# Kernel tuning notes

Hardware: AMD Instinct MI355X
Metric: run time of the kernel (lower is better)

The kernel has to match this reference:

```python
import jax, jax.numpy as jnp
import numpy as np

HEADS, HID, OUT_C, IN_C = 8, 128, 2, 64
D = HID // HEADS
NODE = {"cell0": 50000, "cell1": 100000, "cell2": 25000}
# (src_type, dst_type, edge_name, num_edges)
ETYPES = [("cell0", "cell0", "u00", 200000),
          ("cell1", "cell1", "u11", 200000),
          ("cell1", "cell0", "b10", 100000),
          ("cell2", "cell1", "b21", 50000)]


def _segment_softmax(scores, seg, num_segments):
    # numerically-stable softmax over irregular destination segments
    m = jax.ops.segment_max(scores, seg, num_segments=num_segments)
    e = jnp.exp(scores - m[seg])
    s = jax.ops.segment_sum(e, seg, num_segments=num_segments)
    return e / (s[seg] + 1e-16)


def setup_inputs() -> dict:
    key = jax.random.key(0)
    ks = iter(jax.random.split(key, 64))
    s = 0.1
    inp = {}
    for nt, n in NODE.items():
        inp[f"x_{nt}"] = jax.random.normal(next(ks), (n, IN_C), jnp.float32)
    for st, dt, name, e in ETYPES:
        src = jax.random.randint(next(ks), (e,), 0, NODE[st], jnp.int32)
        dst = jax.random.randint(next(ks), (e,), 0, NODE[dt], jnp.int32)
        inp[f"ei_{name}"] = jnp.stack([src, dst])
    # HANConv params: per node-type projection, per edge-type attention vectors
    for nt in NODE:
        inp[f"W_{nt}"] = jax.random.normal(next(ks), (IN_C, HID), jnp.float32) * s
        inp[f"b_{nt}"] = jnp.zeros((HID,), jnp.float32)
    for _, _, name, _ in ETYPES:
        inp[f"as_{name}"] = jax.random.normal(next(ks), (HEADS, D), jnp.float32) * s
        inp[f"ad_{name}"] = jax.random.normal(next(ks), (HEADS, D), jnp.float32) * s
    # semantic attention params + final classifier
    inp["k_w"] = jax.random.normal(next(ks), (HID, HID), jnp.float32) * s
    inp["k_b"] = jnp.zeros((HID,), jnp.float32)
    inp["q"] = jax.random.normal(next(ks), (HID,), jnp.float32) * s
    inp["lin_w"] = jax.random.normal(next(ks), (HID, OUT_C), jnp.float32) * s
    inp["lin_b"] = jnp.zeros((OUT_C,), jnp.float32)
    return inp


def _han_conv(x, ei, W, b, att_s, att_d, k_w, k_b, q):
    # node-level: project each node type -> [N, H, D]
    h = {nt: (x[nt] @ W[nt] + b[nt]).reshape(-1, HEADS, D) for nt in NODE}
    outs = {nt: [] for nt in NODE}
    for st, dt, name, _ in ETYPES:
        xs, xd = h[st], h[dt]
        a_s = (xs * att_s[name]).sum(-1)  # [Ns, H]
        a_d = (xd * att_d[name]).sum(-1)  # [Nd, H]
        src, dst = ei[name][0], ei[name][1]
        alpha = jax.nn.leaky_relu(a_s[src] + a_d[dst], 0.2)  # [E, H]
        alpha = _segment_softmax(alpha, dst, NODE[dt])
        msg = xs[src] * alpha[:, :, None]  # [E, H, D]
        agg = jax.ops.segment_sum(msg, dst, num_segments=NODE[dt])
        outs[dt].append(jax.nn.relu(agg.reshape(-1, HID)))
    # semantic-level attention across metapaths per dst node type
    res = {}
    for nt, lst in outs.items():
        if not lst:
            res[nt] = None
            continue
        stk = jnp.stack(lst)  # [M, N, HID]
        score = (q * jnp.tanh(stk @ k_w + k_b).mean(1)).sum(-1)  # [M]
        attn = jax.nn.softmax(score)
        res[nt] = jnp.einsum('m,mnf->nf', attn, stk)
    return res


def reference(x_cell0, x_cell1, x_cell2,
              W_cell0, b_cell0, W_cell1, b_cell1, W_cell2, b_cell2,
              as_u00, ad_u00, as_u11, ad_u11, as_b10, ad_b10, as_b21, ad_b21,
              k_w, k_b, q, lin_w, lin_b,
              ei_u00, ei_u11, ei_b10, ei_b21):
    x = {"cell0": x_cell0, "cell1": x_cell1, "cell2": x_cell2}
    ei = {"u00": ei_u00, "u11": ei_u11, "b10": ei_b10, "b21": ei_b21}
    W = {"cell0": W_cell0, "cell1": W_cell1, "cell2": W_cell2}
    b = {"cell0": b_cell0, "cell1": b_cell1, "cell2": b_cell2}
    att_s = {"u00": as_u00, "u11": as_u11, "b10": as_b10, "b21": as_b21}
    att_d = {"u00": ad_u00, "u11": ad_u11, "b10": ad_b10, "b21": ad_b21}
    # HAN.forward calls han_conv twice with identical inputs (first result
    # discarded); in eval mode (dropout off) both calls are identical math,
    # so we compute it once.
    out = _han_conv(x, ei, W, b, att_s, att_d, k_w, k_b, q)
    pooled = sum(jnp.sum(v, axis=0) for v in out.values() if v is not None)  # global_add_pool, batch=None
    return jax.nn.sigmoid(pooled[None, :] @ lin_w + lin_b)  # [1, OUT_C]
```

## Files before the change

### kernel.cpp

```cpp
#include <hip/hip_runtime.h>
#include <hip/hip_fp16.h>

#define N0 50000
#define N1 100000
#define N2 25000
#define E00 200000
#define E11 200000
#define E10 100000
#define E21 50000
#define EE  550000
#define ND  300000
#define NB  293
#define NT_ALL 18750
#define HID 128
#define INC 64

typedef _Float16 half8 __attribute__((ext_vector_type(8)));
typedef _Float16 half4_t __attribute__((ext_vector_type(4)));
typedef float float4v __attribute__((ext_vector_type(4)));
typedef float floatx2 __attribute__((ext_vector_type(2)));

struct PrepT {
    const float* W; const float* bias;
    const float* av0; const float* av1; const float* av2; const float* av3;
    _Float16* wtg; _Float16* adtg; float* bdc;
};

__device__ __forceinline__ void decode_edge(
    int e, const int* ei00, const int* ei10, const int* ei11, const int* ei21,
    int& src, int& slot)
{
    if (e < E00)                    { src = ei00[e];               slot = ei00[E00 + e]; }
    else if (e < E00 + E10)         { int i = e - E00;             src = ei10[i]; slot = 50000  + ei10[E10 + i]; }
    else if (e < E00 + E10 + E11)   { int i = e - E00 - E10;       src = ei11[i]; slot = 100000 + ei11[E11 + i]; }
    else                            { int i = e - E00 - E10 - E11; src = ei21[i]; slot = 200000 + ei21[E21 + i]; }
}

__global__ __launch_bounds__(256) void prep_kernel(
    PrepT p0, PrepT p1, PrepT p2,
    const float* __restrict__ kw, const float* __restrict__ lw,
    unsigned char* __restrict__ kwf8,
    const int* __restrict__ ei00, const int* __restrict__ ei10,
    const int* __restrict__ ei11, const int* __restrict__ ei21,
    int* __restrict__ cnt)
{
    if (blockIdx.x >= 32) {
        int e = (blockIdx.x - 32) * 256 + threadIdx.x;
        if (e >= EE) return;
        int src, slot;
        decode_edge(e, ei00, ei10, ei11, ei21, src, slot);
        atomicAdd(&cnt[slot], 1);
        return;
    }
    if (blockIdx.x >= 24) {
        int base = (blockIdx.x - 24) * 256 + threadIdx.x;
        for (int it = 0; it < 9; ++it) {
            int idx = base + it * 2048;
            int f = idx >> 7, g = idx & 127;
            float v;
            if (f < 128)      v = kw[g * 128 + f];
            else if (f < 130) v = lw[g * 2 + (f - 128)];
            else              v = 0.f;
            int r = __builtin_amdgcn_cvt_pk_fp8_f32(v, 0.f, 0, false);
            kwf8[idx] = (unsigned char)r;
        }
        return;
    }
    PrepT P = (blockIdx.x >= 16) ? p2 : (blockIdx.x >= 8) ? p1 : p0;
    const int lb = blockIdx.x & 7;
    const int t2 = lb * 256 + threadIdx.x;
    {
        int f = t2 >> 4, g0 = (t2 & 15) * 4;
        half4_t v;
#pragma unroll
        for (int j = 0; j < 4; ++j) v[j] = (_Float16)P.W[(g0 + j) * 128 + f];
        *(half4_t*)&P.wtg[f * 64 + g0] = v;
    }
    {
        int c = t2 >> 6, g = t2 & 63;
        const float* av = (c < 8) ? P.av0 : (c < 16) ? P.av1 : (c < 24) ? P.av2 : P.av3;
        float v = 0.f;
        if (av) {
            int hh = c & 7;
#pragma unroll
            for (int d = 0; d < 16; ++d)
                v += P.W[g * 128 + hh * 16 + d] * av[hh * 16 + d];
        }
        P.adtg[c * 64 + g] = (_Float16)v;
    }
    if (lb == 0 && threadIdx.x < 32) {
        int c = threadIdx.x;
        const float* av = (c < 8) ? P.av0 : (c < 16) ? P.av1 : (c < 24) ? P.av2 : P.av3;
        float v = 0.f;
        if (av) {
            int hh = c & 7;
#pragma unroll
            for (int d = 0; d < 16; ++d)
                v += P.bias[hh * 16 + d] * av[hh * 16 + d];
        }
        P.bdc[c] = v;
    }
}

struct PT {
    const float* x; const float* bias; unsigned char* h;
    float* ao0; float* ao1; float* ao2; float* ao3;
    const _Float16* wtg; const _Float16* adtg; const float* bdc;
    int N; int ntiles; int bstart; int nblocks;
};

#define HPAD 136
#define PROJ_BLKS 1024

__global__ __launch_bounds__(256, 2) void proj_mfma(
    PT t0, PT t1, PT t2,
    const int* __restrict__ cnt, int* __restrict__ part)
{
    __shared__ _Float16 ht[4][16][HPAD];
    __shared__ int swt[4];
    const int tid = threadIdx.x;
    const int lane = tid & 63, wv = tid >> 6;
    const int fi = lane & 15, hi = lane >> 4;

    if (blockIdx.x >= PROJ_BLKS) {
        const int b = blockIdx.x - PROJ_BLKS;
        int i0 = b * 1024 + tid * 4;
        int s = 0;
#pragma unroll
        for (int k = 0; k < 4; ++k) { int i = i0 + k; s += (i < ND) ? cnt[i] : 0; }
#pragma unroll
        for (int off = 1; off < 64; off <<= 1) s += __shfl_xor(s, off);
        if ((tid & 63) == 0) swt[tid >> 6] = s;
        __syncthreads();
        if (tid == 0) part[b] = swt[0] + swt[1] + swt[2] + swt[3];
        return;
    }

    PT A = (blockIdx.x >= t2.bstart) ? t2 : (blockIdx.x >= t1.bstart) ? t1 : t0;

    half8 bfr[8][2], bd[2][2];
#pragma unroll
    for (int nt = 0; nt < 8; ++nt)
#pragma unroll
        for (int kb = 0; kb < 2; ++kb)
            bfr[nt][kb] = *(const half8*)&A.wtg[(nt * 16 + fi) * 64 + kb * 32 + hi * 8];
#pragma unroll
    for (int t = 0; t < 2; ++t)
#pragma unroll
        for (int kb = 0; kb < 2; ++kb)
            bd[t][kb] = *(const half8*)&A.adtg[(t * 16 + fi) * 64 + kb * 32 + hi * 8];

    float bvv[8];
#pragma unroll
    for (int nt = 0; nt < 8; ++nt) bvv[nt] = A.bias[nt * 16 + fi];
    const float bdc0 = A.bdc[fi];
    const float bdc1 = A.bdc[16 + fi];

    float* aolo = (fi >= 8) ? A.ao1 : A.ao0;
    float* aohi = (fi >= 8) ? A.ao3 : A.ao2;
    const bool has_hi = (A.ao2 != nullptr) || (A.ao3 != nullptr);

    const int stride = A.nblocks * 4;
    for (int t = (blockIdx.x - A.bstart) * 4 + wv; t < A.ntiles; t += stride) {
        const int base = t * 16;
        int rsrc = base + fi; if (rsrc >= A.N) rsrc = A.N - 1;
        const float* xp = A.x + (size_t)rsrc * 64 + hi * 8;
        float4 u0 = *(const float4*)(xp);
        float4 u1 = *(const float4*)(xp + 4);
        float4 u2 = *(const float4*)(xp + 32);
        float4 u3 = *(const float4*)(xp + 36);
        half8 a0, a1;
        a0[0] = (_Float16)u0.x; a0[1] = (_Float16)u0.y; a0[2] = (_Float16)u0.z; a0[3] = (_Float16)u0.w;
        a0[4] = (_Float16)u1.x; a0[5] = (_Float16)u1.y; a0[6] = (_Float16)u1.z; a0[7] = (_Float16)u1.w;
        a1[0] = (_Float16)u2.x; a1[1] = (_Float16)u2.y; a1[2] = (_Float16)u2.z; a1[3] = (_Float16)u2.w;
        a1[4] = (_Float16)u3.x; a1[5] = (_Float16)u3.y; a1[6] = (_Float16)u3.z; a1[7] = (_Float16)u3.w;

        float4v c[8];
#pragma unroll
        for (int nt = 0; nt < 8; ++nt) {
            float4v z = {0.f, 0.f, 0.f, 0.f};
            z = __builtin_amdgcn_mfma_f32_16x16x32_f16(a0, bfr[nt][0], z, 0, 0, 0);
            z = __builtin_amdgcn_mfma_f32_16x16x32_f16(a1, bfr[nt][1], z, 0, 0, 0);
            c[nt] = z;
        }
        float4v d0 = {0.f, 0.f, 0.f, 0.f};
        d0 = __builtin_amdgcn_mfma_f32_16x16x32_f16(a0, bd[0][0], d0, 0, 0, 0);
        d0 = __builtin_amdgcn_mfma_f32_16x16x32_f16(a1, bd[0][1], d0, 0, 0, 0);
        float4v d1 = {0.f, 0.f, 0.f, 0.f};
        if (has_hi) {
            d1 = __builtin_amdgcn_mfma_f32_16x16x32_f16(a0, bd[1][0], d1, 0, 0, 0);
            d1 = __builtin_amdgcn_mfma_f32_16x16x32_f16(a1, bd[1][1], d1, 0, 0, 0);
        }

#pragma unroll
        for (int nt = 0; nt < 8; ++nt)
#pragma unroll
            for (int r = 0; r < 4; ++r)
                ht[wv][hi * 4 + r][nt * 16 + fi] = (_Float16)(c[nt][r] + bvv[nt]);
#pragma unroll
        for (int i = 0; i < 4; ++i) {
            int row = i * 4 + hi;
            int node = base + row;
            if (node < A.N) {
                half8 v = *(const half8*)&ht[wv][row][fi * 8];
                int pa = __builtin_amdgcn_cvt_pk_fp8_f32((float)v[0], (float)v[1], 0, false);
                pa = __builtin_amdgcn_cvt_pk_fp8_f32((float)v[2], (float)v[3], pa, true);
                int pb = __builtin_amdgcn_cvt_pk_fp8_f32((float)v[4], (float)v[5], 0, false);
                pb = __builtin_amdgcn_cvt_pk_fp8_f32((float)v[6], (float)v[7], pb, true);
                int2 o = {pa, pb};
                *(int2*)(A.h + (size_t)node * 128 + fi * 8) = o;
            }
        }
        if (aolo) {
#pragma unroll
            for (int r = 0; r < 4; ++r) {
                int node = base + hi * 4 + r;
                if (node < A.N) aolo[(size_t)node * 8 + (fi & 7)] = d0[r] + bdc0;
            }
        }
        if (aohi) {
#pragma unroll
            for (int r = 0; r < 4; ++r) {
                int node = base + hi * 4 + r;
                if (node < A.N) aohi[(size_t)node * 8 + (fi & 7)] = d1[r] + bdc1;
            }
        }
    }
}

__global__ __launch_bounds__(256) void scan23_kernel(
    const int* __restrict__ cnt, const int* __restrict__ part,
    int* __restrict__ off, int* __restrict__ cursor)
{
    __shared__ int sd[256];
    __shared__ int pex[512];
    __shared__ int wt[4];
    const int tid = threadIdx.x, b = blockIdx.x;
    const int lane = tid & 63, wv = tid >> 6;

    int p0 = (2 * tid     < NB) ? part[2 * tid]     : 0;
    int p1 = (2 * tid + 1 < NB) ? part[2 * tid + 1] : 0;
    int ps = p0 + p1;
    sd[tid] = ps; __syncthreads();
    for (int d = 1; d < 256; d <<= 1) {
        int v = (tid >= d) ? sd[tid - d] : 0;
        __syncthreads();
        sd[tid] += v;
        __syncthreads();
    }
    int exc = sd[tid] - ps;
    pex[2 * tid] = exc;
    pex[2 * tid + 1] = exc + p0;
    __syncthreads();

    int i0 = b * 1024 + tid * 4;
    int v[4];
#pragma unroll
    for (int k = 0; k < 4; ++k) { int i = i0 + k; v[k] = (i < ND) ? cnt[i] : 0; }
    int ts = v[0] + v[1] + v[2] + v[3];
    int inc = ts;
#pragma unroll
    for (int d = 1; d < 64; d <<= 1) {
        int u = __shfl_up(inc, d);
        if (lane >= d) inc += u;
    }
    int wexc = inc - ts;
    if (lane == 63) wt[wv] = inc;
    __syncthreads();
    int wbase = 0;
    for (int w = 0; w < wv; ++w) wbase += wt[w];
    int base = pex[b] + wbase + wexc;
    int pre = 0;
#pragma unroll
    for (int k = 0; k < 4; ++k) {
        int i = i0 + k;
        if (i < ND) { off[i] = base + pre; cursor[i] = base + pre; }
        pre += v[k];
    }
}

__global__ __launch_bounds__(256) void fill_kernel(
    const int* __restrict__ ei00, const int* __restrict__ ei10,
    const int* __restrict__ ei11, const int* __restrict__ ei21,
    const float* __restrict__ as00, const float* __restrict__ ad00,
    const float* __restrict__ as10, const float* __restrict__ ad10,
    const float* __restrict__ as11, const float* __restrict__ ad11,
    const float* __restrict__ as21, const float* __restrict__ ad21,
    int* __restrict__ cursor, int* __restrict__ srcs, _Float16* __restrict__ wgt)
{
    int e = blockIdx.x * 256 + threadIdx.x;
    if (e >= EE) return;
    int src, d, slot;
    const float* asp; const float* adp;
    if (e < E00) {
        src = ei00[e]; d = ei00[E00 + e]; slot = d; asp = as00; adp = ad00;
    } else if (e < E00 + E10) {
        int i = e - E00; src = ei10[i]; d = ei10[E10 + i]; slot = 50000 + d; asp = as10; adp = ad10;
    } else if (e < E00 + E10 + E11) {
        int i = e - E00 - E10; src = ei11[i]; d = ei11[E11 + i]; slot = 100000 + d; asp = as11; adp = ad11;
    } else {
        int i = e - E00 - E10 - E11; src = ei21[i]; d = ei21[E21 + i]; slot = 200000 + d; asp = as21; adp = ad21;
    }
    float4 sa0 = *(const float4*)(asp + (size_t)src * 8);
    float4 sa1 = *(const float4*)(asp + (size_t)src * 8 + 4);
    float4 da0 = *(const float4*)(adp + (size_t)d * 8);
    float4 da1 = *(const float4*)(adp + (size_t)d * 8 + 4);
    float vv[8] = {sa0.x + da0.x, sa0.y + da0.y, sa0.z + da0.z, sa0.w + da0.w,
                   sa1.x + da1.x, sa1.y + da1.y, sa1.z + da1.z, sa1.w + da1.w};
    half8 w;
#pragma unroll
    for (int h = 0; h < 8; ++h) {
        float v = vv[h];
        v = v > 0.f ? v : 0.2f * v;
        w[h] = (_Float16)__expf(v);
    }
    int pos = atomicAdd(&cursor[slot], 1);
    srcs[pos] = src;
    *(half8*)(wgt + (size_t)pos * 8) = w;
}

__global__ __launch_bounds__(256) void gather_kernel(
    const int* __restrict__ cnt, const int* __restrict__ off,
    const int* __restrict__ srcs, const _Float16* __restrict__ wgt,
    const unsigned char* __restrict__ h0, const unsigned char* __restrict__ h1,
    const unsigned char* __restrict__ h2,
    unsigned char* __restrict__ agg)
{
    const int gid = blockIdx.x * 256 + threadIdx.x;
    const int lane = gid & 63;
    const int g8 = lane >> 3, sub = lane & 7;
    const int slot = (gid >> 6) * 8 + g8;
    const unsigned char* hs = (slot < 50000) ? h0 : (slot < 200000) ? h1 : h2;
    const int deg = cnt[slot], st = off[slot];

    int degm = deg;
    degm = max(degm, __shfl_xor(degm, 8));
    degm = max(degm, __shfl_xor(degm, 16));
    degm = max(degm, __shfl_xor(degm, 32));

    float acc[16];
#pragma unroll
    for (int j = 0; j < 16; ++j) acc[j] = 0.f;
    float sw = 0.f;

    int i = 0;
    for (; i + 2 <= degm; i += 2) {
        bool a0 = (i < deg), a1 = (i + 1 < deg);
        int s0 = 0, s1 = 0;
        if (a0) s0 = srcs[st + i];
        if (a1) s1 = srcs[st + i + 1];
        float w0 = 0.f, w1 = 0.f;
        int4 v0 = {0, 0, 0, 0}, v1 = {0, 0, 0, 0};
        if (a0) { w0 = (float)wgt[(size_t)(st + i) * 8 + sub];
                  v0 = *(const int4*)(hs + (size_t)s0 * 128 + sub * 16); }
        if (a1) { w1 = (float)wgt[(size_t)(st + i + 1) * 8 + sub];
                  v1 = *(const int4*)(hs + (size_t)s1 * 128 + sub * 16); }
        const int wa[4] = {v0.x, v0.y, v0.z, v0.w};
        const int wb[4] = {v1.x, v1.y, v1.z, v1.w};
#pragma unroll
        for (int k = 0; k < 4; ++k) {
            floatx2 fa0 = __builtin_amdgcn_cvt_pk_f32_fp8(wa[k], false);
            floatx2 fa1 = __builtin_amdgcn_cvt_pk_f32_fp8(wa[k], true);
            floatx2 fb0 = __builtin_amdgcn_cvt_pk_f32_fp8(wb[k], false);
            floatx2 fb1 = __builtin_amdgcn_cvt_pk_f32_fp8(wb[k], true);
            acc[4 * k + 0] += w0 * fa0.x + w1 * fb0.x;
            acc[4 * k + 1] += w0 * fa0.y + w1 * fb0.y;
            acc[4 * k + 2] += w0 * fa1.x + w1 * fb1.x;
            acc[4 * k + 3] += w0 * fa1.y + w1 * fb1.y;
        }
        sw += w0 + w1;
    }
    if (i < degm) {
        bool a0 = (i < deg);
        int s0 = 0;
        if (a0) s0 = srcs[st + i];
        float w0 = 0.f;
        int4 v0 = {0, 0, 0, 0};
        if (a0) { w0 = (float)wgt[(size_t)(st + i) * 8 + sub];
                  v0 = *(const int4*)(hs + (size_t)s0 * 128 + sub * 16); }
        const int wa[4] = {v0.x, v0.y, v0.z, v0.w};
#pragma unroll
        for (int k = 0; k < 4; ++k) {
            floatx2 fa0 = __builtin_amdgcn_cvt_pk_f32_fp8(wa[k], false);
            floatx2 fa1 = __builtin_amdgcn_cvt_pk_f32_fp8(wa[k], true);
            acc[4 * k + 0] += w0 * fa0.x;
            acc[4 * k + 1] += w0 * fa0.y;
            acc[4 * k + 2] += w0 * fa1.x;
            acc[4 * k + 3] += w0 * fa1.y;
        }
        sw += w0;
    }

    float rr = __builtin_amdgcn_rcpf(sw + 1e-16f);
    int4 o;
    int pk[4];
#pragma unroll
    for (int k = 0; k < 4; ++k) {
        float r0 = fmaxf(acc[4 * k + 0] * rr, 0.f);
        float r1 = fmaxf(acc[4 * k + 1] * rr, 0.f);
        float r2 = fmaxf(acc[4 * k + 2] * rr, 0.f);
        float r3 = fmaxf(acc[4 * k + 3] * rr, 0.f);
        int p = __builtin_amdgcn_cvt_pk_fp8_f32(r0, r1, 0, false);
        p = __builtin_amdgcn_cvt_pk_fp8_f32(r2, r3, p, true);
        pk[k] = p;
    }
    o.x = pk[0]; o.y = pk[1]; o.z = pk[2]; o.w = pk[3];
    *(int4*)(agg + (size_t)slot * 128 + sub * 16) = o;
}

__global__ __launch_bounds__(256, 2) void semantic_kernel(
    const unsigned char* __restrict__ agg, const unsigned char* __restrict__ kwf8,
    const float* __restrict__ kb, const float* __restrict__ q,
    const float* __restrict__ lb,
    float* __restrict__ cs2, float* __restrict__ score,
    unsigned int* __restrict__ done, float* __restrict__ out)
{
    __shared__ float redv[12];
    const int tid = threadIdx.x;
    const int lane = tid & 63, wv = tid >> 6;
    const int fi = lane & 15, hi = lane >> 4;

    if (tid < 12) redv[tid] = 0.f;
    __syncthreads();

    long bf[9][4];
#pragma unroll
    for (int ft = 0; ft < 9; ++ft)
#pragma unroll
        for (int kk = 0; kk < 4; ++kk)
            bf[ft][kk] = *(const long*)&kwf8[(ft * 16 + fi) * 128 + kk * 32 + hi * 8];

    float qv[8], kbv[8];
#pragma unroll
    for (int ft = 0; ft < 8; ++ft) {
        qv[ft] = q[ft * 16 + fi];
        kbv[ft] = kb[ft * 16 + fi];
    }

    float sc[4] = {0.f, 0.f, 0.f, 0.f};
    float cs[4] = {0.f, 0.f, 0.f, 0.f};
    const int wid = blockIdx.x * 4 + wv;
    const int nw = gridDim.x * 4;

    long af[4] = {0, 0, 0, 0};
    int t = wid;
    if (t < NT_ALL) {
        const unsigned char* rowp = agg + ((size_t)(t * 16 + fi) * 128 + hi * 8);
        af[0] = *(const long*)(rowp);
        af[1] = *(const long*)(rowp + 32);
        af[2] = *(const long*)(rowp + 64);
        af[3] = *(const long*)(rowp + 96);
    }
    while (t < NT_ALL) {
        const int tn = t + nw;
        long afn[4] = {0, 0, 0, 0};
        if (tn < NT_ALL) {
            const unsigned char* rowp = agg + ((size_t)(tn * 16 + fi) * 128 + hi * 8);
            afn[0] = *(const long*)(rowp);
            afn[1] = *(const long*)(rowp + 32);
            afn[2] = *(const long*)(rowp + 64);
            afn[3] = *(const long*)(rowp + 96);
        }
        const int m = (t >= 12500) ? 3 : (t >= 6250) ? 2 : (t >= 3125) ? 1 : 0;
        float tsc = 0.f, tcs;
#pragma unroll
        for (int ft = 0; ft < 8; ++ft) {
            float4v c = {0.f, 0.f, 0.f, 0.f};
            c = __builtin_amdgcn_mfma_f32_16x16x32_fp8_fp8(af[0], bf[ft][0], c, 0, 0, 0);
            c = __builtin_amdgcn_mfma_f32_16x16x32_fp8_fp8(af[1], bf[ft][1], c, 0, 0, 0);
            c = __builtin_amdgcn_mfma_f32_16x16x32_fp8_fp8(af[2], bf[ft][2], c, 0, 0, 0);
            c = __builtin_amdgcn_mfma_f32_16x16x32_fp8_fp8(af[3], bf[ft][3], c, 0, 0, 0);
#pragma unroll
            for (int r = 0; r < 4; ++r) {
                float y = c[r] + kbv[ft];
                float e = __expf(2.f * y);
                tsc += qv[ft] * (1.f - 2.f * __builtin_amdgcn_rcpf(e + 1.f));
            }
        }
        {
            float4v c = {0.f, 0.f, 0.f, 0.f};
            c = __builtin_amdgcn_mfma_f32_16x16x32_fp8_fp8(af[0], bf[8][0], c, 0, 0, 0);
            c = __builtin_amdgcn_mfma_f32_16x16x32_fp8_fp8(af[1], bf[8][1], c, 0, 0, 0);
            c = __builtin_amdgcn_mfma_f32_16x16x32_fp8_fp8(af[2], bf[8][2], c, 0, 0, 0);
            c = __builtin_amdgcn_mfma_f32_16x16x32_fp8_fp8(af[3], bf[8][3], c, 0, 0, 0);
            tcs = c[0] + c[1] + c[2] + c[3];
        }
        if (m == 0)      { sc[0] += tsc; cs[0] += tcs; }
        else if (m == 1) { sc[1] += tsc; cs[1] += tcs; }
        else if (m == 2) { sc[2] += tsc; cs[2] += tcs; }
        else             { sc[3] += tsc; cs[3] += tcs; }
        t = tn;
        af[0] = afn[0]; af[1] = afn[1]; af[2] = afn[2]; af[3] = afn[3];
    }

#pragma unroll
    for (int m = 0; m < 4; ++m) {
        float s = sc[m];
#pragma unroll
        for (int off = 1; off < 64; off <<= 1) s += __shfl_xor(s, off);
        if (lane == 0 && s != 0.f) atomicAdd(&redv[m], s);
        float v = cs[m];
        v += __shfl_xor(v, 16);
        v += __shfl_xor(v, 32);
        if (hi == 0 && fi < 2 && v != 0.f) atomicAdd(&redv[4 + 2 * m + fi], v);
    }
    __syncthreads();
    if (tid < 4)              atomicAdd(&score[tid], redv[tid]);
    if (tid >= 4 && tid < 12) atomicAdd(&cs2[tid - 4], redv[tid]);

    __syncthreads();
    if (tid == 0) {
        __threadfence();
        unsigned int old = atomicAdd(done, 1u);
        if (old == gridDim.x - 1) {
            __threadfence();
            float s0 = score[0] / (float)N0;
            float s1 = score[1] / (float)N0;
            float s2 = score[2] / (float)N1;
            float s3 = score[3] / (float)N1;
            float m0 = fmaxf(s0, s1);
            float e0 = __expf(s0 - m0), e1 = __expf(s1 - m0);
            float a0 = e0 / (e0 + e1), a1 = e1 / (e0 + e1);
            float m1 = fmaxf(s2, s3);
            float e2 = __expf(s2 - m1), e3 = __expf(s3 - m1);
            float a2 = e2 / (e2 + e3), a3 = e3 / (e2 + e3);
            float z0 = a0 * cs2[0] + a1 * cs2[2] + a2 * cs2[4] + a3 * cs2[6] + lb[0];
            float z1 = a0 * cs2[1] + a1 * cs2[3] + a2 * cs2[5] + a3 * cs2[7] + lb[1];
            out[0] = 1.f / (1.f + __expf(-z0));
            out[1] = 1.f / (1.f + __expf(-z1));
        }
    }
}

extern "C" void kernel_launch(void* const* d_in, const int* in_sizes, int n_in,
                              void* d_out, int out_size, void* d_ws, size_t ws_size,
                              hipStream_t stream)
{
    const float* x0  = (const float*)d_in[0];
    const float* x1  = (const float*)d_in[1];
    const float* x2  = (const float*)d_in[2];
    const int* ei00  = (const int*)d_in[3];
    const int* ei11  = (const int*)d_in[4];
    const int* ei10  = (const int*)d_in[5];
    const int* ei21  = (const int*)d_in[6];
    const float* W0  = (const float*)d_in[7];  const float* b0 = (const float*)d_in[8];
    const float* W1  = (const float*)d_in[9];  const float* b1 = (const float*)d_in[10];
    const float* W2  = (const float*)d_in[11]; const float* b2 = (const float*)d_in[12];
    const float* as00 = (const float*)d_in[13]; const float* ad00 = (const float*)d_in[14];
    const float* as11 = (const float*)d_in[15]; const float* ad11 = (const float*)d_in[16];
    const float* as10 = (const float*)d_in[17]; const float* ad10 = (const float*)d_in[18];
    const float* as21 = (const float*)d_in[19]; const float* ad21 = (const float*)d_in[20];
    const float* kw  = (const float*)d_in[21]; const float* kb  = (const float*)d_in[22];
    const float* q   = (const float*)d_in[23];
    const float* lw  = (const float*)d_in[24]; const float* lb  = (const float*)d_in[25];
    float* out = (float*)d_out;

    char* p = (char*)d_ws;
    auto alloc = [&](size_t bytes) {
        char* r = p;
        p += (bytes + 255) & ~(size_t)255;
        return r;
    };
    unsigned char* h0 = (unsigned char*)alloc((size_t)N0 * 128);
    unsigned char* h1 = (unsigned char*)alloc((size_t)N1 * 128);
    unsigned char* h2 = (unsigned char*)alloc((size_t)N2 * 128);
    float* o_as00 = (float*)alloc((size_t)N0 * 32);
    float* o_ad00 = (float*)alloc((size_t)N0 * 32);
    float* o_as11 = (float*)alloc((size_t)N1 * 32);
    float* o_ad11 = (float*)alloc((size_t)N1 * 32);
    float* o_as10 = (float*)alloc((size_t)N1 * 32);
    float* o_ad10 = (float*)alloc((size_t)N0 * 32);
    float* o_as21 = (float*)alloc((size_t)N2 * 32);
    float* o_ad21 = (float*)alloc((size_t)N1 * 32);
    int* off    = (int*)alloc((size_t)ND * 4);
    int* cursor = (int*)alloc((size_t)ND * 4);
    int* part   = (int*)alloc((size_t)512 * 4);
    int* srcs   = (int*)alloc((size_t)EE * 4);
    _Float16* wgt = (_Float16*)alloc((size_t)EE * 16);
    unsigned char* agg = (unsigned char*)alloc((size_t)ND * 128);
    _Float16* wtg0 = (_Float16*)alloc(128 * 64 * 2);
    _Float16* wtg1 = (_Float16*)alloc(128 * 64 * 2);
    _Float16* wtg2 = (_Float16*)alloc(128 * 64 * 2);
    _Float16* adtg0 = (_Float16*)alloc(32 * 64 * 2);
    _Float16* adtg1 = (_Float16*)alloc(32 * 64 * 2);
    _Float16* adtg2 = (_Float16*)alloc(32 * 64 * 2);
    float* bdcg = (float*)alloc(3 * 32 * 4);
    unsigned char* kwf8 = (unsigned char*)alloc(144 * 128);
    char* zstart = p;
    int* cnt = (int*)alloc((size_t)ND * 4);
    float* colsum2 = (float*)alloc(8 * 4);
    float* score   = (float*)alloc(4 * 4);
    unsigned int* done = (unsigned int*)alloc(4);
    size_t zbytes = (size_t)(p - zstart);

    (void)hipMemsetAsync(zstart, 0, zbytes, stream);

    PrepT pp0 = {W0, b0, as00, ad00, ad10, nullptr, wtg0, adtg0, bdcg + 0};
    PrepT pp1 = {W1, b1, as11, ad11, as10, ad21,    wtg1, adtg1, bdcg + 32};
    PrepT pp2 = {W2, b2, as21, nullptr, nullptr, nullptr, wtg2, adtg2, bdcg + 64};
    prep_kernel<<<32 + (EE + 255) / 256, 256, 0, stream>>>(
        pp0, pp1, pp2, kw, lw, kwf8, ei00, ei10, ei11, ei21, cnt);

    PT t0 = {x0, b0, h0,
             o_as00, o_ad00, o_ad10, nullptr,
             wtg0, adtg0, bdcg + 0,
             N0, 3125, 0, 296};
    PT t1 = {x1, b1, h1,
             o_as11, o_ad11, o_as10, o_ad21,
             wtg1, adtg1, bdcg + 32,
             N1, 6250, 296, 584};
    PT t2 = {x2, b2, h2,
             o_as21, nullptr, nullptr, nullptr,
             wtg2, adtg2, bdcg + 64,
             N2, 1563, 880, 144};
    proj_mfma<<<PROJ_BLKS + NB, 256, 0, stream>>>(t0, t1, t2, cnt, part);

    scan23_kernel<<<NB, 256, 0, stream>>>(cnt, part, off, cursor);

    fill_kernel<<<(EE + 255) / 256, 256, 0, stream>>>(ei00, ei10, ei11, ei21,
        o_as00, o_ad00, o_as10, o_ad10, o_as11, o_ad11, o_as21, o_ad21,
        cursor, srcs, wgt);

    gather_kernel<<<ND / 32, 256, 0, stream>>>(cnt, off, srcs, wgt, h0, h1, h2, agg);

    semantic_kernel<<<1024, 256, 0, stream>>>(agg, kwf8, kb, q, lb,
                                              colsum2, score, done, out);
}
```

Measured before the change: 283.1 us.

## Split semantic kernel feature tiles across waves with shared-memory A tiles

The semantic kernel used to have every wave process whole 16-row tiles across all nine feature tiles. It now has each block stage one 16-row fp8 tile in double-buffered, padded shared memory, and each wave computes only 2–3 feature tiles from it. This cuts per-wave register use and the duplicated B-fragment loads. It adds a block barrier on every tile and roughly quarters the rows handled per block, so the grid is doubled to 2048 blocks to compensate.

```diff
diff --git a/kernel.cpp b/kernel.cpp
--- a/kernel.cpp
+++ b/kernel.cpp
@@ -408,6 +408,7 @@
     *(int4*)(agg + (size_t)slot * 128 + sub * 16) = o;
 }
 
+#define ASTR 144
 __global__ __launch_bounds__(256, 2) void semantic_kernel(
     const unsigned char* __restrict__ agg, const unsigned char* __restrict__ kwf8,
     const float* __restrict__ kb, const float* __restrict__ q,
@@ -415,82 +416,90 @@
     float* __restrict__ cs2, float* __restrict__ score,
     unsigned int* __restrict__ done, float* __restrict__ out)
 {
+    __shared__ char abuf[2][16 * ASTR];
     __shared__ float redv[12];
     const int tid = threadIdx.x;
     const int lane = tid & 63, wv = tid >> 6;
     const int fi = lane & 15, hi = lane >> 4;
 
     if (tid < 12) redv[tid] = 0.f;
-    __syncthreads();
-
-    long bf[9][4];
-#pragma unroll
-    for (int ft = 0; ft < 9; ++ft)
-#pragma unroll
-        for (int kk = 0; kk < 4; ++kk)
-            bf[ft][kk] = *(const long*)&kwf8[(ft * 16 + fi) * 128 + kk * 32 + hi * 8];
-
-    float qv[8], kbv[8];
-#pragma unroll
-    for (int ft = 0; ft < 8; ++ft) {
-        qv[ft] = q[ft * 16 + fi];
-        kbv[ft] = kb[ft * 16 + fi];
+
+    const int ftbase = wv * 2;
+    const int nft = (wv == 3) ? 3 : 2;
+
+    long bf[3][4];
+    float qv[3], kbv[3];
+#pragma unroll
+    for (int i = 0; i < 3; ++i) {
+        if (i < nft) {
+            int ft = ftbase + i;
+#pragma unroll
+            for (int kk = 0; kk < 4; ++kk)
+                bf[i][kk] = *(const long*)&kwf8[(ft * 16 + fi) * 128 + kk * 32 + hi * 8];
+            qv[i]  = (ft < 8) ? q[ft * 16 + fi]  : 0.f;
+            kbv[i] = (ft < 8) ? kb[ft * 16 + fi] : 0.f;
+        } else {
+            bf[i][0] = bf[i][1] = bf[i][2] = bf[i][3] = 0;
+            qv[i] = 0.f; kbv[i] = 0.f;
+        }
     }
 
     float sc[4] = {0.f, 0.f, 0.f, 0.f};
     float cs[4] = {0.f, 0.f, 0.f, 0.f};
-    const int wid = blockIdx.x * 4 + wv;
-    const int nw = gridDim.x * 4;
-
-    long af[4] = {0, 0, 0, 0};
-    int t = wid;
+
+    const int s_off = (tid >> 4) * ASTR + (tid & 15) * 8;
+    const int a_off = fi * ASTR + hi * 8;
+
+    int t = blockIdx.x;
+    const int stride = gridDim.x;
     if (t < NT_ALL) {
-        const unsigned char* rowp = agg + ((size_t)(t * 16 + fi) * 128 + hi * 8);
-        af[0] = *(const long*)(rowp);
-        af[1] = *(const long*)(rowp + 32);
-        af[2] = *(const long*)(rowp + 64);
-        af[3] = *(const long*)(rowp + 96);
-    }
+        long areg = *(const long*)(agg + (size_t)t * 2048 + tid * 8);
+        *(long*)&abuf[0][s_off] = areg;
+    }
+    __syncthreads();
+    int cur = 0;
     while (t < NT_ALL) {
-        const int tn = t + nw;
-        long afn[4] = {0, 0, 0, 0};
-        if (tn < NT_ALL) {
-            const unsigned char* rowp = agg + ((size_t)(tn * 16 + fi) * 128 + hi * 8);
-            afn[0] = *(const long*)(rowp);
-            afn[1] = *(const long*)(rowp + 32);
-            afn[2] = *(const long*)(rowp + 64);
-            afn[3] = *(const long*)(rowp + 96);
-        }
+        const int tn = t + stride;
+        long aregn = 0;
+        if (tn < NT_ALL)
+            aregn = *(const long*)(agg + (size_t)tn * 2048 + tid * 8);
+
+        long af[4];
+#pragma unroll
+        for (int kk = 0; kk < 4; ++kk)
+            af[kk] = *(const long*)&abuf[cur][a_off + kk * 32];
+
         const int m = (t >= 12500) ? 3 : (t >= 6250) ? 2 : (t >= 3125) ? 1 : 0;
-        float tsc = 0.f, tcs;
-#pragma unroll
-        for (int ft = 0; ft < 8; ++ft) {
+        float tsc = 0.f, tcs = 0.f;
+#pragma unroll
+        for (int i = 0; i < 3; ++i) {
+            if (i >= nft) continue;
             float4v c = {0.f, 0.f, 0.f, 0.f};
-            c = __builtin_amdgcn_mfma_f32_16x16x32_fp8_fp8(af[0], bf[ft][0], c, 0, 0, 0);
-            c = __builtin_amdgcn_mfma_f32_16x16x32_fp8_fp8(af[1], bf[ft][1], c, 0, 0, 0);
-            c = __builtin_amdgcn_mfma_f32_16x16x32_fp8_fp8(af[2], bf[ft][2], c, 0, 0, 0);
-            c = __builtin_amdgcn_mfma_f32_16x16x32_fp8_fp8(af[3], bf[ft][3], c, 0, 0, 0);
-#pragma unroll
-            for (int r = 0; r < 4; ++r) {
-                float y = c[r] + kbv[ft];
-                float e = __expf(2.f * y);
-                tsc += qv[ft] * (1.f - 2.f * __builtin_amdgcn_rcpf(e + 1.f));
+            c = __builtin_amdgcn_mfma_f32_16x16x32_fp8_fp8(af[0], bf[i][0], c, 0, 0, 0);
+            c = __builtin_amdgcn_mfma_f32_16x16x32_fp8_fp8(af[1], bf[i][1], c, 0, 0, 0);
+            c = __builtin_amdgcn_mfma_f32_16x16x32_fp8_fp8(af[2], bf[i][2], c, 0, 0, 0);
+            c = __builtin_amdgcn_mfma_f32_16x16x32_fp8_fp8(af[3], bf[i][3], c, 0, 0, 0);
+            if (ftbase + i == 8) {
+                tcs = c[0] + c[1] + c[2] + c[3];
+            } else {
+#pragma unroll
+                for (int r = 0; r < 4; ++r) {
+                    float y = c[r] + kbv[i];
+                    float e = __expf(2.f * y);
+                    tsc += qv[i] * (1.f - 2.f * __builtin_amdgcn_rcpf(e + 1.f));
+                }
             }
-        }
-        {
-            float4v c = {0.f, 0.f, 0.f, 0.f};
-            c = __builtin_amdgcn_mfma_f32_16x16x32_fp8_fp8(af[0], bf[8][0], c, 0, 0, 0);
-            c = __builtin_amdgcn_mfma_f32_16x16x32_fp8_fp8(af[1], bf[8][1], c, 0, 0, 0);
-            c = __builtin_amdgcn_mfma_f32_16x16x32_fp8_fp8(af[2], bf[8][2], c, 0, 0, 0);
-            c = __builtin_amdgcn_mfma_f32_16x16x32_fp8_fp8(af[3], bf[8][3], c, 0, 0, 0);
-            tcs = c[0] + c[1] + c[2] + c[3];
         }
         if (m == 0)      { sc[0] += tsc; cs[0] += tcs; }
         else if (m == 1) { sc[1] += tsc; cs[1] += tcs; }
         else if (m == 2) { sc[2] += tsc; cs[2] += tcs; }
         else             { sc[3] += tsc; cs[3] += tcs; }
+
+        if (tn < NT_ALL)
+            *(long*)&abuf[cur ^ 1][s_off] = aregn;
+        __syncthreads();
+        cur ^= 1;
         t = tn;
-        af[0] = afn[0]; af[1] = afn[1]; af[2] = afn[2]; af[3] = afn[3];
     }
 
 #pragma unroll
@@ -623,6 +632,6 @@
 
     gather_kernel<<<ND / 32, 256, 0, stream>>>(cnt, off, srcs, wgt, h0, h1, h2, agg);
 
-    semantic_kernel<<<1024, 256, 0, stream>>>(agg, kwf8, kb, q, lb,
+    semantic_kernel<<<2048, 256, 0, stream>>>(agg, kwf8, kb, q, lb,
                                               colsum2, score, done, out);
 }
```

Result: slower. 301.9 us (+6.6%).
